# Kernel tuning notes

Measured on AMD Instinct MI355X. Metric: run time of the kernel, lower is better.

## Reference

```python
import jax, jax.numpy as jnp
import numpy as np


def setup_inputs() -> dict:
    key = jax.random.key(0)
    kq, kk, kv = jax.random.split(key, 3)
    B, H, S, D = 4, 16, 2048, 64
    q = jax.random.normal(kq, (B, H, S, D), dtype=jnp.float32)
    k = jax.random.normal(kk, (B, H, S, D), dtype=jnp.float32)
    v = jax.random.normal(kv, (B, H, S, D), dtype=jnp.float32)
    return {"q": q, "k": k, "v": v}


def reference(q, k, v):
    # scale = sqrt(d_k); source's self.scale is undefined, standard SDPA scaling assumed
    scale = jnp.asarray(np.sqrt(q.shape[-1]), dtype=q.dtype)
    # [B,H,S,S] scores; sigmoid instead of softmax (no normalization across keys)
    scores = jnp.einsum("bhqd,bhkd->bhqk", q, k) / scale
    attn = jax.nn.sigmoid(scores)
    return jnp.einsum("bhqk,bhkd->bhqd", attn, v)
```

## Files before the change

kernel.cpp:

```cpp
#include <hip/hip_runtime.h>


typedef __bf16 bf16_t;
typedef __attribute__((ext_vector_type(8))) __bf16 bf16x8;
typedef __attribute__((ext_vector_type(4))) __bf16 bf16x4;
typedef __attribute__((ext_vector_type(4))) float  f32x4;

#if defined(__HIP_DEVICE_COMPILE__) && __has_builtin(__builtin_amdgcn_exp2f)
#define FAST_EXP2(x) __builtin_amdgcn_exp2f(x)
#else
#define FAST_EXP2(x) exp2f(x)
#endif
#if defined(__HIP_DEVICE_COMPILE__) && __has_builtin(__builtin_amdgcn_rcpf)
#define FAST_RCP(x) __builtin_amdgcn_rcpf(x)
#else
#define FAST_RCP(x) (1.0f/(x))
#endif

static constexpr int SEQ = 2048;
static constexpr int DH  = 64;
static constexpr int KB  = 32;
static constexpr int NIT = SEQ / KB;
static constexpr int NIT2 = NIT / 2;
static constexpr int QPW = 32;
static constexpr int QPB = 128;
static constexpr int CHUNK = 4096;

__global__ __launch_bounds__(256)
void sigattn_prepass(const float* __restrict__ Kg, const float* __restrict__ Vg,
                     bf16_t* __restrict__ ws)
{
    const int bh = blockIdx.x, it = blockIdx.y;
    const int t  = threadIdx.x;
    const int kb = it * KB;
    const size_t hbase = (size_t)bh * SEQ * DH;
    bf16_t* wbase = ws + ((size_t)bh * NIT + it) * CHUNK;

    {
        const int f = t >> 6, lane = t & 63;
        const int ks = f >> 1, dh = f & 1, c16 = lane & 15, g4 = lane >> 4;
        const float* p = Kg + hbase + (size_t)(kb + ks * 16 + c16) * DH + dh * 32 + g4 * 8;
        f32x4 a = *(const f32x4*)p;
        f32x4 b = *(const f32x4*)(p + 4);
        bf16x8 o;
        o[0] = (bf16_t)a.x; o[1] = (bf16_t)a.y; o[2] = (bf16_t)a.z; o[3] = (bf16_t)a.w;
        o[4] = (bf16_t)b.x; o[5] = (bf16_t)b.y; o[6] = (bf16_t)b.z; o[7] = (bf16_t)b.w;
        *(bf16x8*)&wbase[(size_t)t * 8] = o;
    }
    {
        const int lane = t & 63, dt = t >> 6;
        const int c16 = lane & 15, g4 = lane >> 4;
        const float* p = Vg + hbase + (size_t)kb * DH + dt * 16 + c16;
        bf16x8 o;
        #pragma unroll
        for (int j = 0; j < 8; ++j) {
            const int row = (j >> 2) * 16 + g4 * 4 + (j & 3);
            o[j] = (bf16_t)p[(size_t)row * DH];
        }
        *(bf16x8*)&wbase[2048 + (size_t)t * 8] = o;
    }
}

__global__ __launch_bounds__(256, 4)
void sigattn_main(const float* __restrict__ Qg, const bf16_t* __restrict__ ws,
                  float* __restrict__ Og)
{
    __shared__ __align__(16) bf16_t buf[2][2 * CHUNK];

    const int t    = threadIdx.x;
    const int wave = t >> 6;
    const int lane = t & 63;
    const int c16  = lane & 15;
    const int g4   = lane >> 4;

    const int bh    = blockIdx.x;
    const int qtile = blockIdx.y;

    const float* Qp = Qg + (size_t)bh * SEQ * DH;
    float*       Op = Og + (size_t)bh * SEQ * DH;
    const bf16_t* wsh = ws + (size_t)bh * NIT * CHUNK;

    const int qwave = qtile * QPB + wave * QPW;

    const float qscale = -0.125f * 1.44269504088896340736f;
    bf16x8 qf[2][2];
    #pragma unroll
    for (int qs = 0; qs < 2; ++qs) {
        #pragma unroll
        for (int dh = 0; dh < 2; ++dh) {
            const float* p = Qp + (size_t)(qwave + qs * 16 + c16) * DH + dh * 32 + g4 * 8;
            f32x4 a = *(const f32x4*)p;
            f32x4 b = *(const f32x4*)(p + 4);
            bf16x8 f;
            f[0] = (bf16_t)(a.x * qscale); f[1] = (bf16_t)(a.y * qscale);
            f[2] = (bf16_t)(a.z * qscale); f[3] = (bf16_t)(a.w * qscale);
            f[4] = (bf16_t)(b.x * qscale); f[5] = (bf16_t)(b.y * qscale);
            f[6] = (bf16_t)(b.z * qscale); f[7] = (bf16_t)(b.w * qscale);
            qf[qs][dh] = f;
        }
    }

    bf16x8 rK0, rV0, rK1, rV1;
    auto gload2 = [&](int su) {
        const bf16_t* g = wsh + (size_t)(2 * su) * CHUNK + t * 8;
        rK0 = *(const bf16x8*)g;
        rV0 = *(const bf16x8*)(g + 2048);
        rK1 = *(const bf16x8*)(g + CHUNK);
        rV1 = *(const bf16x8*)(g + CHUNK + 2048);
    };
    auto lstore2 = [&](int nb) {
        *(bf16x8*)&buf[nb][t * 8]                = rK0;
        *(bf16x8*)&buf[nb][2048 + t * 8]         = rV0;
        *(bf16x8*)&buf[nb][CHUNK + t * 8]        = rK1;
        *(bf16x8*)&buf[nb][CHUNK + 2048 + t * 8] = rV1;
    };

    gload2(0);
    lstore2(0);

    f32x4 acc[2][4] = {};

    for (int su = 0; su < NIT2; ++su) {
        const int cur = su & 1;
        __syncthreads();
        if (su + 1 < NIT2) gload2(su + 1);

        #pragma unroll
        for (int h = 0; h < 2; ++h) {
            const bf16_t* base = &buf[cur][h * CHUNK];
            bf16x8 kf[4], vf[4];
            #pragma unroll
            for (int f = 0; f < 4; ++f) kf[f] = *(const bf16x8*)&base[(f * 64 + lane) * 8];
            #pragma unroll
            for (int f = 0; f < 4; ++f) vf[f] = *(const bf16x8*)&base[2048 + (f * 64 + lane) * 8];

            #pragma unroll
            for (int qs = 0; qs < 2; ++qs) {
                f32x4 s0 = {0.f, 0.f, 0.f, 0.f}, s1 = {0.f, 0.f, 0.f, 0.f};
                __builtin_amdgcn_s_setprio(1);
                s0 = __builtin_amdgcn_mfma_f32_16x16x32_bf16(kf[0], qf[qs][0], s0, 0, 0, 0);
                s0 = __builtin_amdgcn_mfma_f32_16x16x32_bf16(kf[1], qf[qs][1], s0, 0, 0, 0);
                s1 = __builtin_amdgcn_mfma_f32_16x16x32_bf16(kf[2], qf[qs][0], s1, 0, 0, 0);
                s1 = __builtin_amdgcn_mfma_f32_16x16x32_bf16(kf[3], qf[qs][1], s1, 0, 0, 0);
                __builtin_amdgcn_s_setprio(0);
                bf16x8 p8;
                #pragma unroll
                for (int r = 0; r < 4; ++r) p8[r]     = (bf16_t)FAST_RCP(1.0f + FAST_EXP2(s0[r]));
                #pragma unroll
                for (int r = 0; r < 4; ++r) p8[4 + r] = (bf16_t)FAST_RCP(1.0f + FAST_EXP2(s1[r]));
                __builtin_amdgcn_s_setprio(1);
                #pragma unroll
                for (int dt = 0; dt < 4; ++dt)
                    acc[qs][dt] = __builtin_amdgcn_mfma_f32_16x16x32_bf16(p8, vf[dt], acc[qs][dt], 0, 0, 0);
                __builtin_amdgcn_s_setprio(0);
            }
        }

        if (su + 1 < NIT2) lstore2(cur ^ 1);
    }

    #pragma unroll
    for (int qs = 0; qs < 2; ++qs) {
        const int q0 = qwave + qs * 16 + g4 * 4;
        #pragma unroll
        for (int r = 0; r < 4; ++r) {
            float* po = Op + (size_t)(q0 + r) * DH + c16;
            po[0]  = acc[qs][0][r];
            po[16] = acc[qs][1][r];
            po[32] = acc[qs][2][r];
            po[48] = acc[qs][3][r];
        }
    }
}

__global__ __launch_bounds__(256, 4)
void sigattn_fallback(const float* __restrict__ Qg, const float* __restrict__ Kg,
                      const float* __restrict__ Vg, float* __restrict__ Og)
{
    __shared__ bf16_t Kbuf[2][4 * 64 * 8];
    __shared__ bf16_t Vbuf[2][4 * 64 * 8];
    const int t = threadIdx.x, wave = t >> 6, lane = t & 63;
    const int c16 = lane & 15, g4 = lane >> 4;
    const int bh = blockIdx.x, qtile = blockIdx.y;
    const size_t hbase = (size_t)bh * SEQ * DH;
    const float* Qp = Qg + hbase; const float* Kp = Kg + hbase;
    const float* Vp = Vg + hbase; float* Op = Og + hbase;
    const int qwave = qtile * QPB + wave * QPW;
    const float qscale = -0.125f * 1.44269504088896340736f;
    bf16x8 qf[2][2];
    #pragma unroll
    for (int qs = 0; qs < 2; ++qs)
        #pragma unroll
        for (int dh = 0; dh < 2; ++dh) {
            const float* p = Qp + (size_t)(qwave + qs * 16 + c16) * DH + dh * 32 + g4 * 8;
            f32x4 a = *(const f32x4*)p; f32x4 b = *(const f32x4*)(p + 4);
            bf16x8 f;
            f[0]=(bf16_t)(a.x*qscale); f[1]=(bf16_t)(a.y*qscale); f[2]=(bf16_t)(a.z*qscale); f[3]=(bf16_t)(a.w*qscale);
            f[4]=(bf16_t)(b.x*qscale); f[5]=(bf16_t)(b.y*qscale); f[6]=(bf16_t)(b.z*qscale); f[7]=(bf16_t)(b.w*qscale);
            qf[qs][dh] = f;
        }
    f32x4 kst0, kst1; float vst[8];
    auto issue_loads = [&](int kb0) {
        const float* pk = Kp + (size_t)(kb0 + (wave >> 1) * 16 + c16) * DH + (wave & 1) * 32 + g4 * 8;
        kst0 = *(const f32x4*)pk; kst1 = *(const f32x4*)(pk + 4);
        const float* pv = Vp + (size_t)(kb0 + g4 * 4) * DH + wave * 16 + c16;
        #pragma unroll
        for (int h = 0; h < 2; ++h)
            #pragma unroll
            for (int j = 0; j < 4; ++j) vst[h * 4 + j] = pv[(size_t)(h * 16 + j) * DH];
    };
    auto store_lds = [&](int buf) {
        bf16x8 k8;
        k8[0]=(bf16_t)kst0.x; k8[1]=(bf16_t)kst0.y; k8[2]=(bf16_t)kst0.z; k8[3]=(bf16_t)kst0.w;
        k8[4]=(bf16_t)kst1.x; k8[5]=(bf16_t)kst1.y; k8[6]=(bf16_t)kst1.z; k8[7]=(bf16_t)kst1.w;
        *(bf16x8*)&Kbuf[buf][t * 8] = k8;
        bf16x8 v8;
        #pragma unroll
        for (int j = 0; j < 8; ++j) v8[j] = (bf16_t)vst[j];
        *(bf16x8*)&Vbuf[buf][t * 8] = v8;
    };
    issue_loads(0); store_lds(0);
    f32x4 acc[2][4] = {};
    for (int it = 0; it < NIT; ++it) {
        const int buf = it & 1;
        __syncthreads();
        if (it + 1 < NIT) issue_loads((it + 1) * KB);
        bf16x8 kf[4], vf[4];
        #pragma unroll
        for (int f = 0; f < 4; ++f) kf[f] = *(const bf16x8*)&Kbuf[buf][(f * 64 + lane) * 8];
        #pragma unroll
        for (int f = 0; f < 4; ++f) vf[f] = *(const bf16x8*)&Vbuf[buf][(f * 64 + lane) * 8];
        #pragma unroll
        for (int qs = 0; qs < 2; ++qs) {
            f32x4 s0 = {0.f,0.f,0.f,0.f}, s1 = {0.f,0.f,0.f,0.f};
            s0 = __builtin_amdgcn_mfma_f32_16x16x32_bf16(kf[0], qf[qs][0], s0, 0, 0, 0);
            s0 = __builtin_amdgcn_mfma_f32_16x16x32_bf16(kf[1], qf[qs][1], s0, 0, 0, 0);
            s1 = __builtin_amdgcn_mfma_f32_16x16x32_bf16(kf[2], qf[qs][0], s1, 0, 0, 0);
            s1 = __builtin_amdgcn_mfma_f32_16x16x32_bf16(kf[3], qf[qs][1], s1, 0, 0, 0);
            bf16x8 p8;
            #pragma unroll
            for (int r = 0; r < 4; ++r) p8[r]     = (bf16_t)FAST_RCP(1.0f + FAST_EXP2(s0[r]));
            #pragma unroll
            for (int r = 0; r < 4; ++r) p8[4 + r] = (bf16_t)FAST_RCP(1.0f + FAST_EXP2(s1[r]));
            #pragma unroll
            for (int dt = 0; dt < 4; ++dt)
                acc[qs][dt] = __builtin_amdgcn_mfma_f32_16x16x32_bf16(p8, vf[dt], acc[qs][dt], 0, 0, 0);
        }
        if (it + 1 < NIT) store_lds(buf ^ 1);
    }
    #pragma unroll
    for (int qs = 0; qs < 2; ++qs) {
        const int q0 = qwave + qs * 16 + g4 * 4;
        #pragma unroll
        for (int r = 0; r < 4; ++r) {
            float* po = Op + (size_t)(q0 + r) * DH + c16;
            po[0]  = acc[qs][0][r];
            po[16] = acc[qs][1][r];
            po[32] = acc[qs][2][r];
            po[48] = acc[qs][3][r];
        }
    }
}

extern "C" void kernel_launch(void* const* d_in, const int* in_sizes, int n_in,
                              void* d_out, int out_size, void* d_ws, size_t ws_size,
                              hipStream_t stream)
{
    const float* q = (const float*)d_in[0];
    const float* k = (const float*)d_in[1];
    const float* v = (const float*)d_in[2];
    float* o = (float*)d_out;
    const size_t need = 64ull * NIT * CHUNK * sizeof(bf16_t);
    if (ws_size >= need) {
        sigattn_prepass<<<dim3(64, NIT), dim3(256), 0, stream>>>(k, v, (bf16_t*)d_ws);
        sigattn_main<<<dim3(64, SEQ / QPB), dim3(256), 0, stream>>>(q, (const bf16_t*)d_ws, o);
    } else {
        sigattn_fallback<<<dim3(64, SEQ / QPB), dim3(256), 0, stream>>>(q, k, v, o);
    }
}
```

Before: 208.3 us.

## Fuse K/V bf16 conversion prepass into main attention kernel

Drops the separate prepass that converted K and V to bf16 in a workspace and has the main kernel load fp32 K/V directly, converting and swizzling into LDS as it goes, two key chunks per stage. This removes one kernel launch and the workspace write and read round trip. In exchange, every query-tile block re-reads and re-converts fp32 K/V, which doubles the global bytes per tile and uses strided scalar V loads. It also keeps more registers live for staging.

After: 219.3 us. +5.3%, slower.

```diff
diff --git a/kernel.cpp b/kernel.cpp
--- a/kernel.cpp
+++ b/kernel.cpp
@@ -3,7 +3,6 @@
 
 typedef __bf16 bf16_t;
 typedef __attribute__((ext_vector_type(8))) __bf16 bf16x8;
-typedef __attribute__((ext_vector_type(4))) __bf16 bf16x4;
 typedef __attribute__((ext_vector_type(4))) float  f32x4;
 
 #if defined(__HIP_DEVICE_COMPILE__) && __has_builtin(__builtin_amdgcn_exp2f)
@@ -26,44 +25,10 @@
 static constexpr int QPB = 128;
 static constexpr int CHUNK = 4096;
 
-__global__ __launch_bounds__(256)
-void sigattn_prepass(const float* __restrict__ Kg, const float* __restrict__ Vg,
-                     bf16_t* __restrict__ ws)
-{
-    const int bh = blockIdx.x, it = blockIdx.y;
-    const int t  = threadIdx.x;
-    const int kb = it * KB;
-    const size_t hbase = (size_t)bh * SEQ * DH;
-    bf16_t* wbase = ws + ((size_t)bh * NIT + it) * CHUNK;
-
-    {
-        const int f = t >> 6, lane = t & 63;
-        const int ks = f >> 1, dh = f & 1, c16 = lane & 15, g4 = lane >> 4;
-        const float* p = Kg + hbase + (size_t)(kb + ks * 16 + c16) * DH + dh * 32 + g4 * 8;
-        f32x4 a = *(const f32x4*)p;
-        f32x4 b = *(const f32x4*)(p + 4);
-        bf16x8 o;
-        o[0] = (bf16_t)a.x; o[1] = (bf16_t)a.y; o[2] = (bf16_t)a.z; o[3] = (bf16_t)a.w;
-        o[4] = (bf16_t)b.x; o[5] = (bf16_t)b.y; o[6] = (bf16_t)b.z; o[7] = (bf16_t)b.w;
-        *(bf16x8*)&wbase[(size_t)t * 8] = o;
-    }
-    {
-        const int lane = t & 63, dt = t >> 6;
-        const int c16 = lane & 15, g4 = lane >> 4;
-        const float* p = Vg + hbase + (size_t)kb * DH + dt * 16 + c16;
-        bf16x8 o;
-        #pragma unroll
-        for (int j = 0; j < 8; ++j) {
-            const int row = (j >> 2) * 16 + g4 * 4 + (j & 3);
-            o[j] = (bf16_t)p[(size_t)row * DH];
-        }
-        *(bf16x8*)&wbase[2048 + (size_t)t * 8] = o;
-    }
-}
 
 __global__ __launch_bounds__(256, 4)
-void sigattn_main(const float* __restrict__ Qg, const bf16_t* __restrict__ ws,
-                  float* __restrict__ Og)
+void sigattn_fused(const float* __restrict__ Qg, const float* __restrict__ Kg,
+                   const float* __restrict__ Vg, float* __restrict__ Og)
 {
     __shared__ __align__(16) bf16_t buf[2][2 * CHUNK];
 
@@ -76,9 +41,11 @@
     const int bh    = blockIdx.x;
     const int qtile = blockIdx.y;
 
-    const float* Qp = Qg + (size_t)bh * SEQ * DH;
-    float*       Op = Og + (size_t)bh * SEQ * DH;
-    const bf16_t* wsh = ws + (size_t)bh * NIT * CHUNK;
+    const size_t hbase = (size_t)bh * SEQ * DH;
+    const float* Qp = Qg + hbase;
+    const float* Kp = Kg + hbase;
+    const float* Vp = Vg + hbase;
+    float*       Op = Og + hbase;
 
     const int qwave = qtile * QPB + wave * QPW;
 
@@ -100,30 +67,50 @@
         }
     }
 
-    bf16x8 rK0, rV0, rK1, rV1;
-    auto gload2 = [&](int su) {
-        const bf16_t* g = wsh + (size_t)(2 * su) * CHUNK + t * 8;
-        rK0 = *(const bf16x8*)g;
-        rV0 = *(const bf16x8*)(g + 2048);
-        rK1 = *(const bf16x8*)(g + CHUNK);
-        rV1 = *(const bf16x8*)(g + CHUNK + 2048);
+    f32x4 kst[2][2];
+    float vst[2][8];
+    auto issue_loads2 = [&](int su) {
+        #pragma unroll
+        for (int c = 0; c < 2; ++c) {
+            const int kb0 = (2 * su + c) * KB;
+            const float* pk = Kp + (size_t)(kb0 + (wave >> 1) * 16 + c16) * DH
+                                 + (wave & 1) * 32 + g4 * 8;
+            kst[c][0] = *(const f32x4*)pk;
+            kst[c][1] = *(const f32x4*)(pk + 4);
+            const float* pv = Vp + (size_t)(kb0 + g4 * 4) * DH + wave * 16 + c16;
+            #pragma unroll
+            for (int h = 0; h < 2; ++h)
+                #pragma unroll
+                for (int j = 0; j < 4; ++j)
+                    vst[c][h * 4 + j] = pv[(size_t)(h * 16 + j) * DH];
+        }
     };
-    auto lstore2 = [&](int nb) {
-        *(bf16x8*)&buf[nb][t * 8]                = rK0;
-        *(bf16x8*)&buf[nb][2048 + t * 8]         = rV0;
-        *(bf16x8*)&buf[nb][CHUNK + t * 8]        = rK1;
-        *(bf16x8*)&buf[nb][CHUNK + 2048 + t * 8] = rV1;
+    auto store2 = [&](int nb) {
+        #pragma unroll
+        for (int c = 0; c < 2; ++c) {
+            bf16x8 k8;
+            #pragma unroll
+            for (int i = 0; i < 4; ++i) {
+                k8[i]     = (bf16_t)kst[c][0][i];
+                k8[4 + i] = (bf16_t)kst[c][1][i];
+            }
+            *(bf16x8*)&buf[nb][c * CHUNK + t * 8] = k8;
+            bf16x8 v8;
+            #pragma unroll
+            for (int j = 0; j < 8; ++j) v8[j] = (bf16_t)vst[c][j];
+            *(bf16x8*)&buf[nb][c * CHUNK + 2048 + t * 8] = v8;
+        }
     };
 
-    gload2(0);
-    lstore2(0);
+    issue_loads2(0);
+    store2(0);
 
     f32x4 acc[2][4] = {};
 
     for (int su = 0; su < NIT2; ++su) {
         const int cur = su & 1;
         __syncthreads();
-        if (su + 1 < NIT2) gload2(su + 1);
+        if (su + 1 < NIT2) issue_loads2(su + 1);
 
         #pragma unroll
         for (int h = 0; h < 2; ++h) {
@@ -156,98 +143,9 @@
             }
         }
 
-        if (su + 1 < NIT2) lstore2(cur ^ 1);
+        if (su + 1 < NIT2) store2(cur ^ 1);
     }
 
-    #pragma unroll
-    for (int qs = 0; qs < 2; ++qs) {
-        const int q0 = qwave + qs * 16 + g4 * 4;
-        #pragma unroll
-        for (int r = 0; r < 4; ++r) {
-            float* po = Op + (size_t)(q0 + r) * DH + c16;
-            po[0]  = acc[qs][0][r];
-            po[16] = acc[qs][1][r];
-            po[32] = acc[qs][2][r];
-            po[48] = acc[qs][3][r];
-        }
-    }
-}
-
-__global__ __launch_bounds__(256, 4)
-void sigattn_fallback(const float* __restrict__ Qg, const float* __restrict__ Kg,
-                      const float* __restrict__ Vg, float* __restrict__ Og)
-{
-    __shared__ bf16_t Kbuf[2][4 * 64 * 8];
-    __shared__ bf16_t Vbuf[2][4 * 64 * 8];
-    const int t = threadIdx.x, wave = t >> 6, lane = t & 63;
-    const int c16 = lane & 15, g4 = lane >> 4;
-    const int bh = blockIdx.x, qtile = blockIdx.y;
-    const size_t hbase = (size_t)bh * SEQ * DH;
-    const float* Qp = Qg + hbase; const float* Kp = Kg + hbase;
-    const float* Vp = Vg + hbase; float* Op = Og + hbase;
-    const int qwave = qtile * QPB + wave * QPW;
-    const float qscale = -0.125f * 1.44269504088896340736f;
-    bf16x8 qf[2][2];
-    #pragma unroll
-    for (int qs = 0; qs < 2; ++qs)
-        #pragma unroll
-        for (int dh = 0; dh < 2; ++dh) {
-            const float* p = Qp + (size_t)(qwave + qs * 16 + c16) * DH + dh * 32 + g4 * 8;
-            f32x4 a = *(const f32x4*)p; f32x4 b = *(const f32x4*)(p + 4);
-            bf16x8 f;
-            f[0]=(bf16_t)(a.x*qscale); f[1]=(bf16_t)(a.y*qscale); f[2]=(bf16_t)(a.z*qscale); f[3]=(bf16_t)(a.w*qscale);
-            f[4]=(bf16_t)(b.x*qscale); f[5]=(bf16_t)(b.y*qscale); f[6]=(bf16_t)(b.z*qscale); f[7]=(bf16_t)(b.w*qscale);
-            qf[qs][dh] = f;
-        }
-    f32x4 kst0, kst1; float vst[8];
-    auto issue_loads = [&](int kb0) {
-        const float* pk = Kp + (size_t)(kb0 + (wave >> 1) * 16 + c16) * DH + (wave & 1) * 32 + g4 * 8;
-        kst0 = *(const f32x4*)pk; kst1 = *(const f32x4*)(pk + 4);
-        const float* pv = Vp + (size_t)(kb0 + g4 * 4) * DH + wave * 16 + c16;
-        #pragma unroll
-        for (int h = 0; h < 2; ++h)
-            #pragma unroll
-            for (int j = 0; j < 4; ++j) vst[h * 4 + j] = pv[(size_t)(h * 16 + j) * DH];
-    };
-    auto store_lds = [&](int buf) {
-        bf16x8 k8;
-        k8[0]=(bf16_t)kst0.x; k8[1]=(bf16_t)kst0.y; k8[2]=(bf16_t)kst0.z; k8[3]=(bf16_t)kst0.w;
-        k8[4]=(bf16_t)kst1.x; k8[5]=(bf16_t)kst1.y; k8[6]=(bf16_t)kst1.z; k8[7]=(bf16_t)kst1.w;
-        *(bf16x8*)&Kbuf[buf][t * 8] = k8;
-        bf16x8 v8;
-        #pragma unroll
-        for (int j = 0; j < 8; ++j) v8[j] = (bf16_t)vst[j];
-        *(bf16x8*)&Vbuf[buf][t * 8] = v8;
-    };
-    issue_loads(0); store_lds(0);
-    f32x4 acc[2][4] = {};
-    for (int it = 0; it < NIT; ++it) {
-        const int buf = it & 1;
-        __syncthreads();
-        if (it + 1 < NIT) issue_loads((it + 1) * KB);
-        bf16x8 kf[4], vf[4];
-        #pragma unroll
-        for (int f = 0; f < 4; ++f) kf[f] = *(const bf16x8*)&Kbuf[buf][(f * 64 + lane) * 8];
-        #pragma unroll
-        for (int f = 0; f < 4; ++f) vf[f] = *(const bf16x8*)&Vbuf[buf][(f * 64 + lane) * 8];
-        #pragma unroll
-        for (int qs = 0; qs < 2; ++qs) {
-            f32x4 s0 = {0.f,0.f,0.f,0.f}, s1 = {0.f,0.f,0.f,0.f};
-            s0 = __builtin_amdgcn_mfma_f32_16x16x32_bf16(kf[0], qf[qs][0], s0, 0, 0, 0);
-            s0 = __builtin_amdgcn_mfma_f32_16x16x32_bf16(kf[1], qf[qs][1], s0, 0, 0, 0);
-            s1 = __builtin_amdgcn_mfma_f32_16x16x32_bf16(kf[2], qf[qs][0], s1, 0, 0, 0);
-            s1 = __builtin_amdgcn_mfma_f32_16x16x32_bf16(kf[3], qf[qs][1], s1, 0, 0, 0);
-            bf16x8 p8;
-            #pragma unroll
-            for (int r = 0; r < 4; ++r) p8[r]     = (bf16_t)FAST_RCP(1.0f + FAST_EXP2(s0[r]));
-            #pragma unroll
-            for (int r = 0; r < 4; ++r) p8[4 + r] = (bf16_t)FAST_RCP(1.0f + FAST_EXP2(s1[r]));
-            #pragma unroll
-            for (int dt = 0; dt < 4; ++dt)
-                acc[qs][dt] = __builtin_amdgcn_mfma_f32_16x16x32_bf16(p8, vf[dt], acc[qs][dt], 0, 0, 0);
-        }
-        if (it + 1 < NIT) store_lds(buf ^ 1);
-    }
     #pragma unroll
     for (int qs = 0; qs < 2; ++qs) {
         const int q0 = qwave + qs * 16 + g4 * 4;
@@ -270,11 +168,6 @@
     const float* k = (const float*)d_in[1];
     const float* v = (const float*)d_in[2];
     float* o = (float*)d_out;
-    const size_t need = 64ull * NIT * CHUNK * sizeof(bf16_t);
-    if (ws_size >= need) {
-        sigattn_prepass<<<dim3(64, NIT), dim3(256), 0, stream>>>(k, v, (bf16_t*)d_ws);
-        sigattn_main<<<dim3(64, SEQ / QPB), dim3(256), 0, stream>>>(q, (const bf16_t*)d_ws, o);
-    } else {
-        sigattn_fallback<<<dim3(64, SEQ / QPB), dim3(256), 0, stream>>>(q, k, v, o);
-    }
+    (void)d_ws; (void)ws_size;
+    sigattn_fused<<<dim3(64, SEQ / QPB), dim3(256), 0, stream>>>(q, k, v, o);
 }
```

## Split main kernel into 8 waves with 16 queries each and shared staging

Applied to the files above, without the earlier changes.

The main kernel now runs 512 threads per block, with each wave owning 16 query rows instead of 32, so per-wave accumulator and Q-fragment registers halve and more waves are resident. Each half of the block loads one of the two K/V chunks into shared memory, so per-thread staging work halves. The V fragment loads are moved after the QK MFMAs to shorten register live ranges. The fallback path is also restructured to process two chunks per barrier. In exchange, each K/V fragment read from shared memory now feeds half as many MFMAs, raising LDS traffic per unit of compute.

After: 296.5 us. 42.4% more time.

```diff
diff --git a/kernel.cpp b/kernel.cpp
--- a/kernel.cpp
+++ b/kernel.cpp
@@ -3,7 +3,6 @@
 
 typedef __bf16 bf16_t;
 typedef __attribute__((ext_vector_type(8))) __bf16 bf16x8;
-typedef __attribute__((ext_vector_type(4))) __bf16 bf16x4;
 typedef __attribute__((ext_vector_type(4))) float  f32x4;
 
 #if defined(__HIP_DEVICE_COMPILE__) && __has_builtin(__builtin_amdgcn_exp2f)
@@ -22,9 +21,10 @@
 static constexpr int KB  = 32;
 static constexpr int NIT = SEQ / KB;
 static constexpr int NIT2 = NIT / 2;
-static constexpr int QPW = 32;
+static constexpr int QPW = 16;
 static constexpr int QPB = 128;
 static constexpr int CHUNK = 4096;
+
 
 __global__ __launch_bounds__(256)
 void sigattn_prepass(const float* __restrict__ Kg, const float* __restrict__ Vg,
@@ -61,7 +61,7 @@
     }
 }
 
-__global__ __launch_bounds__(256, 4)
+__global__ __launch_bounds__(512, 8)
 void sigattn_main(const float* __restrict__ Qg, const bf16_t* __restrict__ ws,
                   float* __restrict__ Og)
 {
@@ -72,6 +72,8 @@
     const int lane = t & 63;
     const int c16  = lane & 15;
     const int g4   = lane >> 4;
+    const int s    = t & 255;
+    const int half = t >> 8;
 
     const int bh    = blockIdx.x;
     const int qtile = blockIdx.y;
@@ -83,93 +85,84 @@
     const int qwave = qtile * QPB + wave * QPW;
 
     const float qscale = -0.125f * 1.44269504088896340736f;
-    bf16x8 qf[2][2];
-    #pragma unroll
-    for (int qs = 0; qs < 2; ++qs) {
-        #pragma unroll
-        for (int dh = 0; dh < 2; ++dh) {
-            const float* p = Qp + (size_t)(qwave + qs * 16 + c16) * DH + dh * 32 + g4 * 8;
-            f32x4 a = *(const f32x4*)p;
-            f32x4 b = *(const f32x4*)(p + 4);
-            bf16x8 f;
-            f[0] = (bf16_t)(a.x * qscale); f[1] = (bf16_t)(a.y * qscale);
-            f[2] = (bf16_t)(a.z * qscale); f[3] = (bf16_t)(a.w * qscale);
-            f[4] = (bf16_t)(b.x * qscale); f[5] = (bf16_t)(b.y * qscale);
-            f[6] = (bf16_t)(b.z * qscale); f[7] = (bf16_t)(b.w * qscale);
-            qf[qs][dh] = f;
-        }
-    }
-
-    bf16x8 rK0, rV0, rK1, rV1;
-    auto gload2 = [&](int su) {
-        const bf16_t* g = wsh + (size_t)(2 * su) * CHUNK + t * 8;
-        rK0 = *(const bf16x8*)g;
-        rV0 = *(const bf16x8*)(g + 2048);
-        rK1 = *(const bf16x8*)(g + CHUNK);
-        rV1 = *(const bf16x8*)(g + CHUNK + 2048);
-    };
-    auto lstore2 = [&](int nb) {
-        *(bf16x8*)&buf[nb][t * 8]                = rK0;
-        *(bf16x8*)&buf[nb][2048 + t * 8]         = rV0;
-        *(bf16x8*)&buf[nb][CHUNK + t * 8]        = rK1;
-        *(bf16x8*)&buf[nb][CHUNK + 2048 + t * 8] = rV1;
-    };
-
-    gload2(0);
-    lstore2(0);
-
-    f32x4 acc[2][4] = {};
+    bf16x8 qf[2];
+    #pragma unroll
+    for (int dh = 0; dh < 2; ++dh) {
+        const float* p = Qp + (size_t)(qwave + c16) * DH + dh * 32 + g4 * 8;
+        f32x4 a = *(const f32x4*)p;
+        f32x4 b = *(const f32x4*)(p + 4);
+        bf16x8 f;
+        f[0] = (bf16_t)(a.x * qscale); f[1] = (bf16_t)(a.y * qscale);
+        f[2] = (bf16_t)(a.z * qscale); f[3] = (bf16_t)(a.w * qscale);
+        f[4] = (bf16_t)(b.x * qscale); f[5] = (bf16_t)(b.y * qscale);
+        f[6] = (bf16_t)(b.z * qscale); f[7] = (bf16_t)(b.w * qscale);
+        qf[dh] = f;
+    }
+
+    bf16x8 rK, rV;
+    auto gload = [&](int su) {
+        const bf16_t* g = wsh + (size_t)(2 * su + half) * CHUNK + s * 8;
+        rK = *(const bf16x8*)g;
+        rV = *(const bf16x8*)(g + 2048);
+    };
+    auto lstore = [&](int nb) {
+        *(bf16x8*)&buf[nb][half * CHUNK + s * 8]        = rK;
+        *(bf16x8*)&buf[nb][half * CHUNK + 2048 + s * 8] = rV;
+    };
+
+    gload(0);
+    lstore(0);
+
+    f32x4 acc[4] = {};
 
     for (int su = 0; su < NIT2; ++su) {
         const int cur = su & 1;
         __syncthreads();
-        if (su + 1 < NIT2) gload2(su + 1);
+        if (su + 1 < NIT2) gload(su + 1);
 
         #pragma unroll
         for (int h = 0; h < 2; ++h) {
             const bf16_t* base = &buf[cur][h * CHUNK];
-            bf16x8 kf[4], vf[4];
+            bf16x8 kf[4];
             #pragma unroll
             for (int f = 0; f < 4; ++f) kf[f] = *(const bf16x8*)&base[(f * 64 + lane) * 8];
+
+            f32x4 s0 = {0.f, 0.f, 0.f, 0.f}, s1 = {0.f, 0.f, 0.f, 0.f};
+            __builtin_amdgcn_s_setprio(1);
+            s0 = __builtin_amdgcn_mfma_f32_16x16x32_bf16(kf[0], qf[0], s0, 0, 0, 0);
+            s0 = __builtin_amdgcn_mfma_f32_16x16x32_bf16(kf[1], qf[1], s0, 0, 0, 0);
+            s1 = __builtin_amdgcn_mfma_f32_16x16x32_bf16(kf[2], qf[0], s1, 0, 0, 0);
+            s1 = __builtin_amdgcn_mfma_f32_16x16x32_bf16(kf[3], qf[1], s1, 0, 0, 0);
+            __builtin_amdgcn_s_setprio(0);
+
+            bf16x8 vf[4];
             #pragma unroll
             for (int f = 0; f < 4; ++f) vf[f] = *(const bf16x8*)&base[2048 + (f * 64 + lane) * 8];
 
-            #pragma unroll
-            for (int qs = 0; qs < 2; ++qs) {
-                f32x4 s0 = {0.f, 0.f, 0.f, 0.f}, s1 = {0.f, 0.f, 0.f, 0.f};
-                __builtin_amdgcn_s_setprio(1);
-                s0 = __builtin_amdgcn_mfma_f32_16x16x32_bf16(kf[0], qf[qs][0], s0, 0, 0, 0);
-                s0 = __builtin_amdgcn_mfma_f32_16x16x32_bf16(kf[1], qf[qs][1], s0, 0, 0, 0);
-                s1 = __builtin_amdgcn_mfma_f32_16x16x32_bf16(kf[2], qf[qs][0], s1, 0, 0, 0);
-                s1 = __builtin_amdgcn_mfma_f32_16x16x32_bf16(kf[3], qf[qs][1], s1, 0, 0, 0);
-                __builtin_amdgcn_s_setprio(0);
-                bf16x8 p8;
-                #pragma unroll
-                for (int r = 0; r < 4; ++r) p8[r]     = (bf16_t)FAST_RCP(1.0f + FAST_EXP2(s0[r]));
-                #pragma unroll
-                for (int r = 0; r < 4; ++r) p8[4 + r] = (bf16_t)FAST_RCP(1.0f + FAST_EXP2(s1[r]));
-                __builtin_amdgcn_s_setprio(1);
-                #pragma unroll
-                for (int dt = 0; dt < 4; ++dt)
-                    acc[qs][dt] = __builtin_amdgcn_mfma_f32_16x16x32_bf16(p8, vf[dt], acc[qs][dt], 0, 0, 0);
-                __builtin_amdgcn_s_setprio(0);
-            }
-        }
-
-        if (su + 1 < NIT2) lstore2(cur ^ 1);
-    }
-
-    #pragma unroll
-    for (int qs = 0; qs < 2; ++qs) {
-        const int q0 = qwave + qs * 16 + g4 * 4;
-        #pragma unroll
-        for (int r = 0; r < 4; ++r) {
-            float* po = Op + (size_t)(q0 + r) * DH + c16;
-            po[0]  = acc[qs][0][r];
-            po[16] = acc[qs][1][r];
-            po[32] = acc[qs][2][r];
-            po[48] = acc[qs][3][r];
-        }
+            bf16x8 p8;
+            #pragma unroll
+            for (int r = 0; r < 4; ++r) p8[r]     = (bf16_t)FAST_RCP(1.0f + FAST_EXP2(s0[r]));
+            #pragma unroll
+            for (int r = 0; r < 4; ++r) p8[4 + r] = (bf16_t)FAST_RCP(1.0f + FAST_EXP2(s1[r]));
+
+            __builtin_amdgcn_s_setprio(1);
+            #pragma unroll
+            for (int dt = 0; dt < 4; ++dt)
+                acc[dt] = __builtin_amdgcn_mfma_f32_16x16x32_bf16(p8, vf[dt], acc[dt], 0, 0, 0);
+            __builtin_amdgcn_s_setprio(0);
+        }
+
+        if (su + 1 < NIT2) lstore(cur ^ 1);
+    }
+
+    const int q0 = qwave + g4 * 4;
+    #pragma unroll
+    for (int r = 0; r < 4; ++r) {
+        float* po = Op + (size_t)(q0 + r) * DH + c16;
+        po[0]  = acc[0][r];
+        po[16] = acc[1][r];
+        po[32] = acc[2][r];
+        po[48] = acc[3][r];
     }
 }
 
@@ -177,15 +170,14 @@
 void sigattn_fallback(const float* __restrict__ Qg, const float* __restrict__ Kg,
                       const float* __restrict__ Vg, float* __restrict__ Og)
 {
-    __shared__ bf16_t Kbuf[2][4 * 64 * 8];
-    __shared__ bf16_t Vbuf[2][4 * 64 * 8];
+    __shared__ __align__(16) bf16_t buf[2][2 * CHUNK];
     const int t = threadIdx.x, wave = t >> 6, lane = t & 63;
     const int c16 = lane & 15, g4 = lane >> 4;
     const int bh = blockIdx.x, qtile = blockIdx.y;
     const size_t hbase = (size_t)bh * SEQ * DH;
     const float* Qp = Qg + hbase; const float* Kp = Kg + hbase;
     const float* Vp = Vg + hbase; float* Op = Og + hbase;
-    const int qwave = qtile * QPB + wave * QPW;
+    const int qwave = qtile * QPB + wave * 32;
     const float qscale = -0.125f * 1.44269504088896340736f;
     bf16x8 qf[2][2];
     #pragma unroll
@@ -199,54 +191,65 @@
             f[4]=(bf16_t)(b.x*qscale); f[5]=(bf16_t)(b.y*qscale); f[6]=(bf16_t)(b.z*qscale); f[7]=(bf16_t)(b.w*qscale);
             qf[qs][dh] = f;
         }
-    f32x4 kst0, kst1; float vst[8];
-    auto issue_loads = [&](int kb0) {
-        const float* pk = Kp + (size_t)(kb0 + (wave >> 1) * 16 + c16) * DH + (wave & 1) * 32 + g4 * 8;
-        kst0 = *(const f32x4*)pk; kst1 = *(const f32x4*)(pk + 4);
-        const float* pv = Vp + (size_t)(kb0 + g4 * 4) * DH + wave * 16 + c16;
-        #pragma unroll
-        for (int h = 0; h < 2; ++h)
-            #pragma unroll
-            for (int j = 0; j < 4; ++j) vst[h * 4 + j] = pv[(size_t)(h * 16 + j) * DH];
-    };
-    auto store_lds = [&](int buf) {
-        bf16x8 k8;
-        k8[0]=(bf16_t)kst0.x; k8[1]=(bf16_t)kst0.y; k8[2]=(bf16_t)kst0.z; k8[3]=(bf16_t)kst0.w;
-        k8[4]=(bf16_t)kst1.x; k8[5]=(bf16_t)kst1.y; k8[6]=(bf16_t)kst1.z; k8[7]=(bf16_t)kst1.w;
-        *(bf16x8*)&Kbuf[buf][t * 8] = k8;
-        bf16x8 v8;
-        #pragma unroll
-        for (int j = 0; j < 8; ++j) v8[j] = (bf16_t)vst[j];
-        *(bf16x8*)&Vbuf[buf][t * 8] = v8;
-    };
-    issue_loads(0); store_lds(0);
+    f32x4 kst[2][2]; float vst[2][8];
+    auto issue_loads2 = [&](int su) {
+        #pragma unroll
+        for (int c = 0; c < 2; ++c) {
+            const int kb0 = (2 * su + c) * KB;
+            const float* pk = Kp + (size_t)(kb0 + (wave >> 1) * 16 + c16) * DH + (wave & 1) * 32 + g4 * 8;
+            kst[c][0] = *(const f32x4*)pk; kst[c][1] = *(const f32x4*)(pk + 4);
+            const float* pv = Vp + (size_t)(kb0 + g4 * 4) * DH + wave * 16 + c16;
+            #pragma unroll
+            for (int h = 0; h < 2; ++h)
+                #pragma unroll
+                for (int j = 0; j < 4; ++j) vst[c][h * 4 + j] = pv[(size_t)(h * 16 + j) * DH];
+        }
+    };
+    auto store2 = [&](int nb) {
+        #pragma unroll
+        for (int c = 0; c < 2; ++c) {
+            bf16x8 k8;
+            #pragma unroll
+            for (int i = 0; i < 4; ++i) { k8[i] = (bf16_t)kst[c][0][i]; k8[4+i] = (bf16_t)kst[c][1][i]; }
+            *(bf16x8*)&buf[nb][c * CHUNK + t * 8] = k8;
+            bf16x8 v8;
+            #pragma unroll
+            for (int j = 0; j < 8; ++j) v8[j] = (bf16_t)vst[c][j];
+            *(bf16x8*)&buf[nb][c * CHUNK + 2048 + t * 8] = v8;
+        }
+    };
+    issue_loads2(0); store2(0);
     f32x4 acc[2][4] = {};
-    for (int it = 0; it < NIT; ++it) {
-        const int buf = it & 1;
+    for (int su = 0; su < NIT2; ++su) {
+        const int cur = su & 1;
         __syncthreads();
-        if (it + 1 < NIT) issue_loads((it + 1) * KB);
-        bf16x8 kf[4], vf[4];
-        #pragma unroll
-        for (int f = 0; f < 4; ++f) kf[f] = *(const bf16x8*)&Kbuf[buf][(f * 64 + lane) * 8];
-        #pragma unroll
-        for (int f = 0; f < 4; ++f) vf[f] = *(const bf16x8*)&Vbuf[buf][(f * 64 + lane) * 8];
-        #pragma unroll
-        for (int qs = 0; qs < 2; ++qs) {
-            f32x4 s0 = {0.f,0.f,0.f,0.f}, s1 = {0.f,0.f,0.f,0.f};
-            s0 = __builtin_amdgcn_mfma_f32_16x16x32_bf16(kf[0], qf[qs][0], s0, 0, 0, 0);
-            s0 = __builtin_amdgcn_mfma_f32_16x16x32_bf16(kf[1], qf[qs][1], s0, 0, 0, 0);
-            s1 = __builtin_amdgcn_mfma_f32_16x16x32_bf16(kf[2], qf[qs][0], s1, 0, 0, 0);
-            s1 = __builtin_amdgcn_mfma_f32_16x16x32_bf16(kf[3], qf[qs][1], s1, 0, 0, 0);
-            bf16x8 p8;
-            #pragma unroll
-            for (int r = 0; r < 4; ++r) p8[r]     = (bf16_t)FAST_RCP(1.0f + FAST_EXP2(s0[r]));
-            #pragma unroll
-            for (int r = 0; r < 4; ++r) p8[4 + r] = (bf16_t)FAST_RCP(1.0f + FAST_EXP2(s1[r]));
-            #pragma unroll
-            for (int dt = 0; dt < 4; ++dt)
-                acc[qs][dt] = __builtin_amdgcn_mfma_f32_16x16x32_bf16(p8, vf[dt], acc[qs][dt], 0, 0, 0);
-        }
-        if (it + 1 < NIT) store_lds(buf ^ 1);
+        if (su + 1 < NIT2) issue_loads2(su + 1);
+        #pragma unroll
+        for (int h = 0; h < 2; ++h) {
+            const bf16_t* base = &buf[cur][h * CHUNK];
+            bf16x8 kf[4], vf[4];
+            #pragma unroll
+            for (int f = 0; f < 4; ++f) kf[f] = *(const bf16x8*)&base[(f * 64 + lane) * 8];
+            #pragma unroll
+            for (int f = 0; f < 4; ++f) vf[f] = *(const bf16x8*)&base[2048 + (f * 64 + lane) * 8];
+            #pragma unroll
+            for (int qs = 0; qs < 2; ++qs) {
+                f32x4 s0 = {0.f,0.f,0.f,0.f}, s1 = {0.f,0.f,0.f,0.f};
+                s0 = __builtin_amdgcn_mfma_f32_16x16x32_bf16(kf[0], qf[qs][0], s0, 0, 0, 0);
+                s0 = __builtin_amdgcn_mfma_f32_16x16x32_bf16(kf[1], qf[qs][1], s0, 0, 0, 0);
+                s1 = __builtin_amdgcn_mfma_f32_16x16x32_bf16(kf[2], qf[qs][0], s1, 0, 0, 0);
+                s1 = __builtin_amdgcn_mfma_f32_16x16x32_bf16(kf[3], qf[qs][1], s1, 0, 0, 0);
+                bf16x8 p8;
+                #pragma unroll
+                for (int r = 0; r < 4; ++r) p8[r]     = (bf16_t)FAST_RCP(1.0f + FAST_EXP2(s0[r]));
+                #pragma unroll
+                for (int r = 0; r < 4; ++r) p8[4 + r] = (bf16_t)FAST_RCP(1.0f + FAST_EXP2(s1[r]));
+                #pragma unroll
+                for (int dt = 0; dt < 4; ++dt)
+                    acc[qs][dt] = __builtin_amdgcn_mfma_f32_16x16x32_bf16(p8, vf[dt], acc[qs][dt], 0, 0, 0);
+            }
+        }
+        if (su + 1 < NIT2) store2(cur ^ 1);
     }
     #pragma unroll
     for (int qs = 0; qs < 2; ++qs) {
@@ -273,7 +276,7 @@
     const size_t need = 64ull * NIT * CHUNK * sizeof(bf16_t);
     if (ws_size >= need) {
         sigattn_prepass<<<dim3(64, NIT), dim3(256), 0, stream>>>(k, v, (bf16_t*)d_ws);
-        sigattn_main<<<dim3(64, SEQ / QPB), dim3(256), 0, stream>>>(q, (const bf16_t*)d_ws, o);
+        sigattn_main<<<dim3(64, SEQ / QPB), dim3(512), 0, stream>>>(q, (const bf16_t*)d_ws, o);
     } else {
         sigattn_fallback<<<dim3(64, SEQ / QPB), dim3(256), 0, stream>>>(q, k, v, o);
     }
```

## Read prepacked K/V fragments directly from global memory, dropping LDS staging

Applied to the files above, without the earlier changes.

The main kernel stops staging prepacked bf16 K/V chunks through double-buffered shared memory and has each wave load its MFMA fragments straight from the workspace, which is expected to hit in L2/L1. This removes the __syncthreads barriers and the LDS writes and reads, at the cost of every wave issuing its own global loads with exposed latency, partly hidden by unroll 2. The fallback kernel is restructured to use the earlier two-chunk LDS scheme, but it only runs when the workspace is too small.

Result: no change. 210.8 us (+1.2%).

```diff
diff --git a/kernel.cpp b/kernel.cpp
--- a/kernel.cpp
+++ b/kernel.cpp
@@ -3,7 +3,6 @@
 
 typedef __bf16 bf16_t;
 typedef __attribute__((ext_vector_type(8))) __bf16 bf16x8;
-typedef __attribute__((ext_vector_type(4))) __bf16 bf16x4;
 typedef __attribute__((ext_vector_type(4))) float  f32x4;
 
 #if defined(__HIP_DEVICE_COMPILE__) && __has_builtin(__builtin_amdgcn_exp2f)
@@ -21,10 +20,10 @@
 static constexpr int DH  = 64;
 static constexpr int KB  = 32;
 static constexpr int NIT = SEQ / KB;
-static constexpr int NIT2 = NIT / 2;
 static constexpr int QPW = 32;
 static constexpr int QPB = 128;
 static constexpr int CHUNK = 4096;
+
 
 __global__ __launch_bounds__(256)
 void sigattn_prepass(const float* __restrict__ Kg, const float* __restrict__ Vg,
@@ -65,8 +64,6 @@
 void sigattn_main(const float* __restrict__ Qg, const bf16_t* __restrict__ ws,
                   float* __restrict__ Og)
 {
-    __shared__ __align__(16) bf16_t buf[2][2 * CHUNK];
-
     const int t    = threadIdx.x;
     const int wave = t >> 6;
     const int lane = t & 63;
@@ -100,63 +97,39 @@
         }
     }
 
-    bf16x8 rK0, rV0, rK1, rV1;
-    auto gload2 = [&](int su) {
-        const bf16_t* g = wsh + (size_t)(2 * su) * CHUNK + t * 8;
-        rK0 = *(const bf16x8*)g;
-        rV0 = *(const bf16x8*)(g + 2048);
-        rK1 = *(const bf16x8*)(g + CHUNK);
-        rV1 = *(const bf16x8*)(g + CHUNK + 2048);
-    };
-    auto lstore2 = [&](int nb) {
-        *(bf16x8*)&buf[nb][t * 8]                = rK0;
-        *(bf16x8*)&buf[nb][2048 + t * 8]         = rV0;
-        *(bf16x8*)&buf[nb][CHUNK + t * 8]        = rK1;
-        *(bf16x8*)&buf[nb][CHUNK + 2048 + t * 8] = rV1;
-    };
-
-    gload2(0);
-    lstore2(0);
+    const bf16_t* lbase = wsh + (size_t)lane * 8;
 
     f32x4 acc[2][4] = {};
 
-    for (int su = 0; su < NIT2; ++su) {
-        const int cur = su & 1;
-        __syncthreads();
-        if (su + 1 < NIT2) gload2(su + 1);
-
-        #pragma unroll
-        for (int h = 0; h < 2; ++h) {
-            const bf16_t* base = &buf[cur][h * CHUNK];
-            bf16x8 kf[4], vf[4];
-            #pragma unroll
-            for (int f = 0; f < 4; ++f) kf[f] = *(const bf16x8*)&base[(f * 64 + lane) * 8];
-            #pragma unroll
-            for (int f = 0; f < 4; ++f) vf[f] = *(const bf16x8*)&base[2048 + (f * 64 + lane) * 8];
-
-            #pragma unroll
-            for (int qs = 0; qs < 2; ++qs) {
-                f32x4 s0 = {0.f, 0.f, 0.f, 0.f}, s1 = {0.f, 0.f, 0.f, 0.f};
-                __builtin_amdgcn_s_setprio(1);
-                s0 = __builtin_amdgcn_mfma_f32_16x16x32_bf16(kf[0], qf[qs][0], s0, 0, 0, 0);
-                s0 = __builtin_amdgcn_mfma_f32_16x16x32_bf16(kf[1], qf[qs][1], s0, 0, 0, 0);
-                s1 = __builtin_amdgcn_mfma_f32_16x16x32_bf16(kf[2], qf[qs][0], s1, 0, 0, 0);
-                s1 = __builtin_amdgcn_mfma_f32_16x16x32_bf16(kf[3], qf[qs][1], s1, 0, 0, 0);
-                __builtin_amdgcn_s_setprio(0);
-                bf16x8 p8;
-                #pragma unroll
-                for (int r = 0; r < 4; ++r) p8[r]     = (bf16_t)FAST_RCP(1.0f + FAST_EXP2(s0[r]));
-                #pragma unroll
-                for (int r = 0; r < 4; ++r) p8[4 + r] = (bf16_t)FAST_RCP(1.0f + FAST_EXP2(s1[r]));
-                __builtin_amdgcn_s_setprio(1);
-                #pragma unroll
-                for (int dt = 0; dt < 4; ++dt)
-                    acc[qs][dt] = __builtin_amdgcn_mfma_f32_16x16x32_bf16(p8, vf[dt], acc[qs][dt], 0, 0, 0);
-                __builtin_amdgcn_s_setprio(0);
-            }
-        }
-
-        if (su + 1 < NIT2) lstore2(cur ^ 1);
+    #pragma unroll 2
+    for (int it = 0; it < NIT; ++it) {
+        const bf16_t* cb = lbase + (size_t)it * CHUNK;
+        bf16x8 kf[4], vf[4];
+        #pragma unroll
+        for (int f = 0; f < 4; ++f) kf[f] = *(const bf16x8*)&cb[(size_t)f * 64 * 8];
+        #pragma unroll
+        for (int f = 0; f < 4; ++f) vf[f] = *(const bf16x8*)&cb[2048 + (size_t)f * 64 * 8];
+
+        #pragma unroll
+        for (int qs = 0; qs < 2; ++qs) {
+            f32x4 s0 = {0.f, 0.f, 0.f, 0.f}, s1 = {0.f, 0.f, 0.f, 0.f};
+            __builtin_amdgcn_s_setprio(1);
+            s0 = __builtin_amdgcn_mfma_f32_16x16x32_bf16(kf[0], qf[qs][0], s0, 0, 0, 0);
+            s0 = __builtin_amdgcn_mfma_f32_16x16x32_bf16(kf[1], qf[qs][1], s0, 0, 0, 0);
+            s1 = __builtin_amdgcn_mfma_f32_16x16x32_bf16(kf[2], qf[qs][0], s1, 0, 0, 0);
+            s1 = __builtin_amdgcn_mfma_f32_16x16x32_bf16(kf[3], qf[qs][1], s1, 0, 0, 0);
+            __builtin_amdgcn_s_setprio(0);
+            bf16x8 p8;
+            #pragma unroll
+            for (int r = 0; r < 4; ++r) p8[r]     = (bf16_t)FAST_RCP(1.0f + FAST_EXP2(s0[r]));
+            #pragma unroll
+            for (int r = 0; r < 4; ++r) p8[4 + r] = (bf16_t)FAST_RCP(1.0f + FAST_EXP2(s1[r]));
+            __builtin_amdgcn_s_setprio(1);
+            #pragma unroll
+            for (int dt = 0; dt < 4; ++dt)
+                acc[qs][dt] = __builtin_amdgcn_mfma_f32_16x16x32_bf16(p8, vf[dt], acc[qs][dt], 0, 0, 0);
+            __builtin_amdgcn_s_setprio(0);
+        }
     }
 
     #pragma unroll
@@ -177,15 +150,14 @@
 void sigattn_fallback(const float* __restrict__ Qg, const float* __restrict__ Kg,
                       const float* __restrict__ Vg, float* __restrict__ Og)
 {
-    __shared__ bf16_t Kbuf[2][4 * 64 * 8];
-    __shared__ bf16_t Vbuf[2][4 * 64 * 8];
+    __shared__ __align__(16) bf16_t buf[2][2 * CHUNK];
     const int t = threadIdx.x, wave = t >> 6, lane = t & 63;
     const int c16 = lane & 15, g4 = lane >> 4;
     const int bh = blockIdx.x, qtile = blockIdx.y;
     const size_t hbase = (size_t)bh * SEQ * DH;
     const float* Qp = Qg + hbase; const float* Kp = Kg + hbase;
     const float* Vp = Vg + hbase; float* Op = Og + hbase;
-    const int qwave = qtile * QPB + wave * QPW;
+    const int qwave = qtile * QPB + wave * 32;
     const float qscale = -0.125f * 1.44269504088896340736f;
     bf16x8 qf[2][2];
     #pragma unroll
@@ -199,54 +171,65 @@
             f[4]=(bf16_t)(b.x*qscale); f[5]=(bf16_t)(b.y*qscale); f[6]=(bf16_t)(b.z*qscale); f[7]=(bf16_t)(b.w*qscale);
             qf[qs][dh] = f;
         }
-    f32x4 kst0, kst1; float vst[8];
-    auto issue_loads = [&](int kb0) {
-        const float* pk = Kp + (size_t)(kb0 + (wave >> 1) * 16 + c16) * DH + (wave & 1) * 32 + g4 * 8;
-        kst0 = *(const f32x4*)pk; kst1 = *(const f32x4*)(pk + 4);
-        const float* pv = Vp + (size_t)(kb0 + g4 * 4) * DH + wave * 16 + c16;
-        #pragma unroll
-        for (int h = 0; h < 2; ++h)
-            #pragma unroll
-            for (int j = 0; j < 4; ++j) vst[h * 4 + j] = pv[(size_t)(h * 16 + j) * DH];
+    f32x4 kst[2][2]; float vst[2][8];
+    auto issue_loads2 = [&](int su) {
+        #pragma unroll
+        for (int c = 0; c < 2; ++c) {
+            const int kb0 = (2 * su + c) * KB;
+            const float* pk = Kp + (size_t)(kb0 + (wave >> 1) * 16 + c16) * DH + (wave & 1) * 32 + g4 * 8;
+            kst[c][0] = *(const f32x4*)pk; kst[c][1] = *(const f32x4*)(pk + 4);
+            const float* pv = Vp + (size_t)(kb0 + g4 * 4) * DH + wave * 16 + c16;
+            #pragma unroll
+            for (int h = 0; h < 2; ++h)
+                #pragma unroll
+                for (int j = 0; j < 4; ++j) vst[c][h * 4 + j] = pv[(size_t)(h * 16 + j) * DH];
+        }
     };
-    auto store_lds = [&](int buf) {
-        bf16x8 k8;
-        k8[0]=(bf16_t)kst0.x; k8[1]=(bf16_t)kst0.y; k8[2]=(bf16_t)kst0.z; k8[3]=(bf16_t)kst0.w;
-        k8[4]=(bf16_t)kst1.x; k8[5]=(bf16_t)kst1.y; k8[6]=(bf16_t)kst1.z; k8[7]=(bf16_t)kst1.w;
-        *(bf16x8*)&Kbuf[buf][t * 8] = k8;
-        bf16x8 v8;
-        #pragma unroll
-        for (int j = 0; j < 8; ++j) v8[j] = (bf16_t)vst[j];
-        *(bf16x8*)&Vbuf[buf][t * 8] = v8;
+    auto store2 = [&](int nb) {
+        #pragma unroll
+        for (int c = 0; c < 2; ++c) {
+            bf16x8 k8;
+            #pragma unroll
+            for (int i = 0; i < 4; ++i) { k8[i] = (bf16_t)kst[c][0][i]; k8[4+i] = (bf16_t)kst[c][1][i]; }
+            *(bf16x8*)&buf[nb][c * CHUNK + t * 8] = k8;
+            bf16x8 v8;
+            #pragma unroll
+            for (int j = 0; j < 8; ++j) v8[j] = (bf16_t)vst[c][j];
+            *(bf16x8*)&buf[nb][c * CHUNK + 2048 + t * 8] = v8;
+        }
     };
-    issue_loads(0); store_lds(0);
+    issue_loads2(0); store2(0);
     f32x4 acc[2][4] = {};
-    for (int it = 0; it < NIT; ++it) {
-        const int buf = it & 1;
+    for (int su = 0; su < NIT / 2; ++su) {
+        const int cur = su & 1;
         __syncthreads();
-        if (it + 1 < NIT) issue_loads((it + 1) * KB);
-        bf16x8 kf[4], vf[4];
-        #pragma unroll
-        for (int f = 0; f < 4; ++f) kf[f] = *(const bf16x8*)&Kbuf[buf][(f * 64 + lane) * 8];
-        #pragma unroll
-        for (int f = 0; f < 4; ++f) vf[f] = *(const bf16x8*)&Vbuf[buf][(f * 64 + lane) * 8];
-        #pragma unroll
-        for (int qs = 0; qs < 2; ++qs) {
-            f32x4 s0 = {0.f,0.f,0.f,0.f}, s1 = {0.f,0.f,0.f,0.f};
-            s0 = __builtin_amdgcn_mfma_f32_16x16x32_bf16(kf[0], qf[qs][0], s0, 0, 0, 0);
-            s0 = __builtin_amdgcn_mfma_f32_16x16x32_bf16(kf[1], qf[qs][1], s0, 0, 0, 0);
-            s1 = __builtin_amdgcn_mfma_f32_16x16x32_bf16(kf[2], qf[qs][0], s1, 0, 0, 0);
-            s1 = __builtin_amdgcn_mfma_f32_16x16x32_bf16(kf[3], qf[qs][1], s1, 0, 0, 0);
-            bf16x8 p8;
-            #pragma unroll
-            for (int r = 0; r < 4; ++r) p8[r]     = (bf16_t)FAST_RCP(1.0f + FAST_EXP2(s0[r]));
-            #pragma unroll
-            for (int r = 0; r < 4; ++r) p8[4 + r] = (bf16_t)FAST_RCP(1.0f + FAST_EXP2(s1[r]));
-            #pragma unroll
-            for (int dt = 0; dt < 4; ++dt)
-                acc[qs][dt] = __builtin_amdgcn_mfma_f32_16x16x32_bf16(p8, vf[dt], acc[qs][dt], 0, 0, 0);
-        }
-        if (it + 1 < NIT) store_lds(buf ^ 1);
+        if (su + 1 < NIT / 2) issue_loads2(su + 1);
+        #pragma unroll
+        for (int h = 0; h < 2; ++h) {
+            const bf16_t* base = &buf[cur][h * CHUNK];
+            bf16x8 kf[4], vf[4];
+            #pragma unroll
+            for (int f = 0; f < 4; ++f) kf[f] = *(const bf16x8*)&base[(f * 64 + lane) * 8];
+            #pragma unroll
+            for (int f = 0; f < 4; ++f) vf[f] = *(const bf16x8*)&base[2048 + (f * 64 + lane) * 8];
+            #pragma unroll
+            for (int qs = 0; qs < 2; ++qs) {
+                f32x4 s0 = {0.f,0.f,0.f,0.f}, s1 = {0.f,0.f,0.f,0.f};
+                s0 = __builtin_amdgcn_mfma_f32_16x16x32_bf16(kf[0], qf[qs][0], s0, 0, 0, 0);
+                s0 = __builtin_amdgcn_mfma_f32_16x16x32_bf16(kf[1], qf[qs][1], s0, 0, 0, 0);
+                s1 = __builtin_amdgcn_mfma_f32_16x16x32_bf16(kf[2], qf[qs][0], s1, 0, 0, 0);
+                s1 = __builtin_amdgcn_mfma_f32_16x16x32_bf16(kf[3], qf[qs][1], s1, 0, 0, 0);
+                bf16x8 p8;
+                #pragma unroll
+                for (int r = 0; r < 4; ++r) p8[r]     = (bf16_t)FAST_RCP(1.0f + FAST_EXP2(s0[r]));
+                #pragma unroll
+                for (int r = 0; r < 4; ++r) p8[4 + r] = (bf16_t)FAST_RCP(1.0f + FAST_EXP2(s1[r]));
+                #pragma unroll
+                for (int dt = 0; dt < 4; ++dt)
+                    acc[qs][dt] = __builtin_amdgcn_mfma_f32_16x16x32_bf16(p8, vf[dt], acc[qs][dt], 0, 0, 0);
+            }
+        }
+        if (su + 1 < NIT / 2) store2(cur ^ 1);
     }
     #pragma unroll
     for (int qs = 0; qs < 2; ++qs) {
@@ -275,6 +258,6 @@
         sigattn_prepass<<<dim3(64, NIT), dim3(256), 0, stream>>>(k, v, (bf16_t*)d_ws);
         sigattn_main<<<dim3(64, SEQ / QPB), dim3(256), 0, stream>>>(q, (const bf16_t*)d_ws, o);
     } else {
-        sigattn_fallback<<<dim3(64, SEQ / QPB), dim3(256), 0, stream>>>(q, k, v, o);
-    }
-}
+        sigattn_fallback<<<dim3(64, SEQ / 128), dim3(256), 0, stream>>>(q, k, v, o);
+    }
+}
```
